# Optimization experiments

Hardware: AMD Instinct MI355X
Metric: run time of the kernel (lower is better)

Reference implementation:

```python
import jax, jax.numpy as jnp
import numpy as np

N, L, K = 2048, 256, 16

def setup_inputs() -> dict:
    rng = np.random.default_rng(0)
    # per level: wavelet index = l (distinct across levels), plus K-1 random distinct rest indices
    sel = np.zeros((L, K), dtype=np.int64)
    wav = np.arange(L, dtype=np.int64)
    all_idx = np.arange(N)
    for l in range(L):
        others = rng.choice(np.delete(all_idx, l), size=K - 1, replace=False)
        sel[l] = np.sort(np.concatenate([[l], others]))
    key = jax.random.key(0)
    k1, k2 = jax.random.split(key)
    M = jax.random.normal(k1, (N, N), dtype=jnp.float32)
    A = 0.5 * (M + M.T)  # symmetric matrix, as MMF expects
    O_all = jax.random.normal(k2, (L, K, K), dtype=jnp.float32) / np.float32(K) ** 0.5
    return {"A": A, "O_all": O_all, "sel_idx": jnp.asarray(sel), "wav_idx": jnp.asarray(wav)}


def reference(A, O_all, sel_idx, wav_idx):
    # Torch builds a dense NxN U = eye with O scattered into the KxK block at
    # sel_idx x sel_idx, then A <- U A U^T and right <- U @ right.
    # Equivalent efficient form: only the K selected rows/cols change.
    n = A.shape[0]

    def step(carry, xs):
        A, right = carry
        O, idx = xs  # O: (K,K), idx: (K,)
        A = A.at[idx].set(O @ A[idx])              # U @ A   : rewrite K rows
        A = A.at[:, idx].set(A[:, idx] @ O.T)      # ... @ U^T: rewrite K cols
        right = right.at[idx].set(O @ right[idx])  # right <- U @ right
        return (A, right), None

    right0 = jnp.eye(n, dtype=A.dtype)
    (A_f, right), _ = jax.lax.scan(step, (A, right0), (O_all, sel_idx))

    # final_active_index: 1 everywhere except wavelet indices
    active = jnp.ones((n,), dtype=A.dtype).at[wav_idx].set(0.0)
    # left_index = eye - diag(diag(outer)) + outer  -> diag all ones, off-diag = a_i*a_j
    left = jnp.outer(active, active)
    left = left.at[jnp.diag_indices(n)].set(1.0)
    D = A_f * left
    A_rec = right.T @ D @ right
    return (A_rec, right, D)
```

## Files before the change

kernel.cpp:

```cpp
#include <hip/hip_runtime.h>

#define N 2048
#define LEV 256
#define KS 16

typedef __attribute__((ext_vector_type(8))) short bfx8;
typedef __attribute__((ext_vector_type(4))) float fx4;
typedef unsigned short u16;
typedef unsigned int u32;

static const size_t NN = (size_t)N * N;

__device__ inline u16 bf16_rne(float f) {
    u32 u = __builtin_bit_cast(u32, f);
    u32 r = (u + 0x7FFFu + ((u >> 16) & 1u)) >> 16;
    return (u16)r;
}
__device__ inline float bf16_f(u16 h) {
    u32 u = ((u32)h) << 16;
    return __builtin_bit_cast(float, u);
}

#define GLDS16(gp, lp) __builtin_amdgcn_global_load_lds( \
    (const __attribute__((address_space(1))) void*)(uintptr_t)(gp), \
    (__attribute__((address_space(3))) void*)(u32)(uintptr_t)(lp), 16, 0, 0)

__device__ inline float qadd(float x) {
#if __has_builtin(__builtin_amdgcn_mov_dpp)
    int a = __builtin_amdgcn_mov_dpp(__builtin_bit_cast(int, x), 0xB1, 0xF, 0xF, true);
    float y = x + __builtin_bit_cast(float, a);
    int b = __builtin_amdgcn_mov_dpp(__builtin_bit_cast(int, y), 0x4E, 0xF, 0xF, true);
    return y + __builtin_bit_cast(float, b);
#else
    float y = x + __shfl_xor(x, 1);
    return y + __shfl_xor(y, 2);
#endif
}

__global__ __launch_bounds__(64)
void front_k(const float* __restrict__ O_all, const int* __restrict__ sel,
             float* __restrict__ RT, const float* __restrict__ A,
             u16* __restrict__ a2h) {
    __shared__ float x[2048];
    const int lane = threadIdx.x;

    if (blockIdx.x >= 2048) {
        u16* a2l = a2h + NN;
        size_t p = (((size_t)blockIdx.x - 2048) * 64 + lane) * 8;
        float4 v0 = *(const float4*)(A + p);
        float4 v1 = *(const float4*)(A + p + 4);
        float vv[8] = {v0.x, v0.y, v0.z, v0.w, v1.x, v1.y, v1.z, v1.w};
        bfx8 hs, ls;
        #pragma unroll
        for (int i = 0; i < 8; ++i) {
            u16 h = bf16_rne(vv[i]);
            hs[i] = (short)h;
            ls[i] = (short)bf16_rne(vv[i] - bf16_f(h));
        }
        *(bfx8*)(a2h + p) = hs;
        *(bfx8*)(a2l + p) = ls;
        return;
    }

    const int i    = lane >> 2;
    const int kg   = lane & 3;
    const int col  = blockIdx.x;

    const float4 z = make_float4(0.f, 0.f, 0.f, 0.f);
    #pragma unroll
    for (int q = 0; q < 8; ++q) *(float4*)&x[q * 256 + lane * 4] = z;
    if (lane == 0) x[col] = 1.0f;

    const float* obase = O_all + i * KS + kg * 4;
    const int*   gbase = sel + kg * 4;

#define CMP(f, g, wv) { \
    float p = f.x * x[g.x] + f.y * x[g.y] + f.z * x[g.z] + f.w * x[g.w]; \
    p = qadd(p); \
    if (kg == 0) x[wv] = p; }

    float4 f0 = *(const float4*)(obase);
    int4   g0 = *(const int4*)(gbase);
    int    w0 = sel[i];
    float4 f1 = *(const float4*)(obase + 256);
    int4   g1 = *(const int4*)(gbase + KS);
    int    w1 = sel[KS + i];

    for (int l = 0; l < LEV; l += 2) {
        float4 f2, f3; int4 g2, g3; int w2, w3;
        if (l + 2 < LEV) {
            f2 = *(const float4*)(obase + (size_t)(l + 2) * 256);
            g2 = *(const int4*)(gbase + (l + 2) * KS);
            w2 = sel[(l + 2) * KS + i];
            f3 = *(const float4*)(obase + (size_t)(l + 3) * 256);
            g3 = *(const int4*)(gbase + (l + 3) * KS);
            w3 = sel[(l + 3) * KS + i];
        } else { f2 = f0; g2 = g0; w2 = w0; f3 = f1; g3 = g1; w3 = w1; }

        CMP(f0, g0, w0)
        CMP(f1, g1, w1)
        f0 = f2; g0 = g2; w0 = w2;
        f1 = f3; g1 = g3; w1 = w3;
    }
#undef CMP

    #pragma unroll
    for (int q = 0; q < 8; ++q)
        *(float4*)&RT[(size_t)col * N + q * 256 + lane * 4] =
            *(const float4*)&x[q * 256 + lane * 4];
}

__global__ __launch_bounds__(256)
void split_rt_k(const float* __restrict__ RT, u16* __restrict__ r2h,
                u16* __restrict__ rth, float* __restrict__ Rrm) {
    __shared__ float t[64][65];
    u16* r2l = r2h + NN;
    u16* rtl = rth + NN;
    const int r0 = (blockIdx.x >> 5) * 64, c0 = (blockIdx.x & 31) * 64;
    #pragma unroll
    for (int i = 0; i < 16; ++i) {
        int q = i * 256 + threadIdx.x;
        int rr = q >> 6, cc = q & 63;
        t[rr][cc] = RT[(size_t)(r0 + rr) * N + c0 + cc];
    }
    __syncthreads();
    #pragma unroll
    for (int i = 0; i < 16; ++i) {
        int q = i * 256 + threadIdx.x;
        int rr = q >> 6, cc = q & 63;
        float v = t[rr][cc];
        u16 h = bf16_rne(v);
        size_t po = (size_t)(r0 + rr) * N + c0 + cc;
        rth[po] = h;
        rtl[po] = bf16_rne(v - bf16_f(h));
        float w = t[cc][rr];
        u16 h2 = bf16_rne(w);
        size_t pt = (size_t)(c0 + rr) * N + r0 + cc;
        r2h[pt] = h2;
        r2l[pt] = bf16_rne(w - bf16_f(h2));
        Rrm[pt] = w;
    }
}

__global__ __launch_bounds__(256)
void unsplit_k(const u16* __restrict__ hi, float* __restrict__ dst) {
    const u16* lo = hi + NN;
    size_t p = ((size_t)blockIdx.x * 256 + threadIdx.x) * 8;
    bfx8 hs = *(const bfx8*)(hi + p);
    bfx8 ls = *(const bfx8*)(lo + p);
    float4 o0, o1;
    o0.x = bf16_f((u16)hs[0]) + bf16_f((u16)ls[0]);
    o0.y = bf16_f((u16)hs[1]) + bf16_f((u16)ls[1]);
    o0.z = bf16_f((u16)hs[2]) + bf16_f((u16)ls[2]);
    o0.w = bf16_f((u16)hs[3]) + bf16_f((u16)ls[3]);
    o1.x = bf16_f((u16)hs[4]) + bf16_f((u16)ls[4]);
    o1.y = bf16_f((u16)hs[5]) + bf16_f((u16)ls[5]);
    o1.z = bf16_f((u16)hs[6]) + bf16_f((u16)ls[6]);
    o1.w = bf16_f((u16)hs[7]) + bf16_f((u16)ls[7]);
    *(float4*)(dst + p)     = o0;
    *(float4*)(dst + p + 4) = o1;
}

template<int MASKED, int OMODE>
__global__ __launch_bounds__(256)
void gemm_bf3(const u16* __restrict__ Xp, const u16* __restrict__ Yp,
              float* __restrict__ Cf, u16* __restrict__ Cs,
              const int* __restrict__ wav, int Lw) {
    __shared__ __align__(16) u16 sm[24576];
    __shared__ float rowf[128], colf[64];

    const int tid = threadIdx.x;
    const int xcd = blockIdx.x & 7, idx = blockIdx.x >> 3;
    const int sup = 4 * xcd + (idx >> 4);
    const int wi4 = idx & 15;
    const int by = (sup >> 3) * 4 + (wi4 >> 2);
    const int bx = (sup & 7) * 4 + (wi4 & 3);
    const int i0 = by * 128, j0 = bx * 64;
    const int lane = tid & 63, w = tid >> 6;
    const int wm = (w >> 1) * 64, wn = (w & 1) * 32;
    const int fr = lane & 15;

    if (MASKED) {
        if (tid < 128) rowf[tid] = 1.0f;
        if (tid >= 128 && tid < 192) colf[tid - 128] = 1.0f;
        __syncthreads();
        for (int t = tid; t < Lw; t += 256) {
            int wv = wav[t];
            int dr = wv - i0; if (0 <= dr && dr < 128) rowf[dr] = 0.0f;
            int dc = wv - j0; if (0 <= dc && dc < 64)  colf[dc] = 0.0f;
        }
    }

    fx4 acc[4][2];
    #pragma unroll
    for (int m = 0; m < 4; ++m)
        #pragma unroll
        for (int n = 0; n < 2; ++n)
            acc[m][n] = (fx4)0.0f;

    const u16* Xh = Xp; const u16* Xl = Xp + NN;
    const u16* Yh = Yp; const u16* Yl = Yp + NN;

    const int rl   = lane >> 3;
    const int gcol = ((lane & 7) ^ rl) << 3;
    const int wq   = w * 1024;

    #define STAGE(kt) { \
        const int k0s = (kt) * 64; \
        char* lb0 = (char*)sm + wq; \
        _Pragma("unroll") \
        for (int q = 0; q < 4; ++q) { \
            const int row = q * 32 + w * 8 + rl; \
            const size_t xo = (size_t)(i0 + row) * N + k0s + gcol; \
            GLDS16(Xh + xo, lb0 + q * 4096); \
            GLDS16(Xl + xo, lb0 + 16384 + q * 4096); \
        } \
        _Pragma("unroll") \
        for (int q = 0; q < 2; ++q) { \
            const int row = q * 32 + w * 8 + rl; \
            const size_t yo = (size_t)(j0 + row) * N + k0s + gcol; \
            GLDS16(Yh + yo, lb0 + 32768 + q * 4096); \
            GLDS16(Yl + yo, lb0 + 40960 + q * 4096); \
        } }

    const int kq  = (lane >> 4) << 4;
    const int frx = (fr & 7) << 4;

    #define COMPUTE() { \
        const char* base = (const char*)sm; \
        _Pragma("unroll") \
        for (int s = 0; s < 2; ++s) { \
            const int cb = s * 64 + kq; \
            bfx8 ah[4], al[4]; \
            _Pragma("unroll") \
            for (int m = 0; m < 4; ++m) { \
                const int off = (wm + m * 16 + fr) * 128 + (cb ^ frx); \
                ah[m] = *(const bfx8*)(base + off); \
                al[m] = *(const bfx8*)(base + 16384 + off); \
            } \
            _Pragma("unroll") \
            for (int n = 0; n < 2; ++n) { \
                const int off = (wn + n * 16 + fr) * 128 + (cb ^ frx); \
                bfx8 bh = *(const bfx8*)(base + 32768 + off); \
                bfx8 bl = *(const bfx8*)(base + 40960 + off); \
                _Pragma("unroll") \
                for (int m = 0; m < 4; ++m) { \
                    acc[m][n] = __builtin_amdgcn_mfma_f32_16x16x32_bf16(ah[m], bh, acc[m][n], 0, 0, 0); \
                    acc[m][n] = __builtin_amdgcn_mfma_f32_16x16x32_bf16(ah[m], bl, acc[m][n], 0, 0, 0); \
                    acc[m][n] = __builtin_amdgcn_mfma_f32_16x16x32_bf16(al[m], bh, acc[m][n], 0, 0, 0); \
                } \
            } \
        } }

    constexpr int NT = N / 64;
    for (int kt = 0; kt < NT; ++kt) {
        STAGE(kt)
        __syncthreads();
        COMPUTE()
        __syncthreads();
    }

    const int crow0 = (lane >> 4) * 4;
    #pragma unroll
    for (int m = 0; m < 4; ++m) {
        #pragma unroll
        for (int n = 0; n < 2; ++n) {
            #pragma unroll
            for (int r = 0; r < 4; ++r) {
                const int li = wm + m * 16 + crow0 + r;
                const int lj = wn + n * 16 + fr;
                float v = acc[m][n][r];
                if (MASKED) {
                    if (i0 + li != j0 + lj) v *= rowf[li] * colf[lj];
                }
                const size_t off = (size_t)(i0 + li) * N + j0 + lj;
                if (OMODE == 0) {
                    Cf[off] = v;
                } else {
                    u16 h = bf16_rne(v);
                    Cs[off]      = h;
                    Cs[NN + off] = bf16_rne(v - bf16_f(h));
                }
            }
        }
    }
    #undef STAGE
    #undef COMPUTE
}

extern "C" void kernel_launch(void* const* d_in, const int* in_sizes, int n_in,
                              void* d_out, int out_size, void* d_ws, size_t ws_size,
                              hipStream_t stream) {
    const float* A     = (const float*)d_in[0];
    const float* O_all = (const float*)d_in[1];
    const int*   sel   = (const int*)d_in[2];
    const int*   wav   = (const int*)d_in[3];
    const int    Lw    = in_sizes[3];

    float* O1 = (float*)d_out;
    float* O2 = O1 + NN;
    float* O3 = O1 + 2 * NN;

    u16*   W1u = (u16*)d_ws;
    u16*   W2u = (u16*)((char*)d_ws + 2 * NN * sizeof(u16));
    u16*   O1u = (u16*)O1;
    u16*   O3u = (u16*)O3;

    const int SGRID = (int)(NN / (256 * 8));

    front_k<<<2048 + (int)(NN / (64 * 8)), 64, 0, stream>>>(O_all, sel, O3, A, W2u);
    split_rt_k<<<(N / 64) * (N / 64), 256, 0, stream>>>(O3, O1u, W1u, O2);

    gemm_bf3<0, 1><<<512, 256, 0, stream>>>(O1u, W2u, nullptr, O3u, nullptr, 0);
    gemm_bf3<1, 1><<<512, 256, 0, stream>>>(O3u, O1u, nullptr, W2u, wav, Lw);
    gemm_bf3<0, 1><<<512, 256, 0, stream>>>(W1u, W2u, nullptr, O3u, nullptr, 0);
    gemm_bf3<0, 0><<<512, 256, 0, stream>>>(O3u, W1u, O1, nullptr, nullptr, 0);
    unsplit_k<<<SGRID, 256, 0, stream>>>(W2u, O3);
}
```

Before: 265.4 us.

## Load GEMM B operand directly to registers and split RT in front kernel

The GEMM kernel stops staging the Y (B) operand through LDS and has each lane load its MFMA B fragments straight from global memory into registers, which shrinks LDS use and removes the LDS write/read traffic for B. Separately, the bf16 hi/lo split of RT moves into the front kernel's final store, so split_rt_k only writes the transposed outputs. The direct global loads for B are 16-byte per-lane reads spread across 16 rows and are issued before the barrier. They may expose more latency and fetch the same data redundantly across waves that share B columns.

```diff
diff --git a/kernel.cpp b/kernel.cpp
--- a/kernel.cpp
+++ b/kernel.cpp
@@ -39,8 +39,8 @@
 
 __global__ __launch_bounds__(64)
 void front_k(const float* __restrict__ O_all, const int* __restrict__ sel,
-             float* __restrict__ RT, const float* __restrict__ A,
-             u16* __restrict__ a2h) {
+             float* __restrict__ RT, u16* __restrict__ rth,
+             const float* __restrict__ A, u16* __restrict__ a2h) {
     __shared__ float x[2048];
     const int lane = threadIdx.x;
 
@@ -104,18 +104,29 @@
     }
 #undef CMP
 
-    #pragma unroll
-    for (int q = 0; q < 8; ++q)
-        *(float4*)&RT[(size_t)col * N + q * 256 + lane * 4] =
-            *(const float4*)&x[q * 256 + lane * 4];
+    u16* rtl = rth + NN;
+    #pragma unroll
+    for (int q = 0; q < 8; ++q) {
+        float4 v = *(const float4*)&x[q * 256 + lane * 4];
+        *(float4*)&RT[(size_t)col * N + q * 256 + lane * 4] = v;
+        float vv[4] = {v.x, v.y, v.z, v.w};
+        u16 hh[4], ll[4];
+        #pragma unroll
+        for (int e = 0; e < 4; ++e) {
+            hh[e] = bf16_rne(vv[e]);
+            ll[e] = bf16_rne(vv[e] - bf16_f(hh[e]));
+        }
+        const size_t po = (size_t)col * N + q * 256 + lane * 4;
+        *(ushort4*)(rth + po) = make_ushort4(hh[0], hh[1], hh[2], hh[3]);
+        *(ushort4*)(rtl + po) = make_ushort4(ll[0], ll[1], ll[2], ll[3]);
+    }
 }
 
 __global__ __launch_bounds__(256)
 void split_rt_k(const float* __restrict__ RT, u16* __restrict__ r2h,
-                u16* __restrict__ rth, float* __restrict__ Rrm) {
+                float* __restrict__ Rrm) {
     __shared__ float t[64][65];
     u16* r2l = r2h + NN;
-    u16* rtl = rth + NN;
     const int r0 = (blockIdx.x >> 5) * 64, c0 = (blockIdx.x & 31) * 64;
     #pragma unroll
     for (int i = 0; i < 16; ++i) {
@@ -128,11 +139,6 @@
     for (int i = 0; i < 16; ++i) {
         int q = i * 256 + threadIdx.x;
         int rr = q >> 6, cc = q & 63;
-        float v = t[rr][cc];
-        u16 h = bf16_rne(v);
-        size_t po = (size_t)(r0 + rr) * N + c0 + cc;
-        rth[po] = h;
-        rtl[po] = bf16_rne(v - bf16_f(h));
         float w = t[cc][rr];
         u16 h2 = bf16_rne(w);
         size_t pt = (size_t)(c0 + rr) * N + r0 + cc;
@@ -166,7 +172,7 @@
 void gemm_bf3(const u16* __restrict__ Xp, const u16* __restrict__ Yp,
               float* __restrict__ Cf, u16* __restrict__ Cs,
               const int* __restrict__ wav, int Lw) {
-    __shared__ __align__(16) u16 sm[24576];
+    __shared__ __align__(16) u16 sm[16384];
     __shared__ float rowf[128], colf[64];
 
     const int tid = threadIdx.x;
@@ -179,6 +185,7 @@
     const int lane = tid & 63, w = tid >> 6;
     const int wm = (w >> 1) * 64, wn = (w & 1) * 32;
     const int fr = lane & 15;
+    const int fk = (lane >> 4) * 8;
 
     if (MASKED) {
         if (tid < 128) rowf[tid] = 1.0f;
@@ -199,64 +206,62 @@
             acc[m][n] = (fx4)0.0f;
 
     const u16* Xh = Xp; const u16* Xl = Xp + NN;
-    const u16* Yh = Yp; const u16* Yl = Yp + NN;
 
     const int rl   = lane >> 3;
     const int gcol = ((lane & 7) ^ rl) << 3;
     const int wq   = w * 1024;
-
-    #define STAGE(kt) { \
-        const int k0s = (kt) * 64; \
-        char* lb0 = (char*)sm + wq; \
-        _Pragma("unroll") \
-        for (int q = 0; q < 4; ++q) { \
-            const int row = q * 32 + w * 8 + rl; \
-            const size_t xo = (size_t)(i0 + row) * N + k0s + gcol; \
-            GLDS16(Xh + xo, lb0 + q * 4096); \
-            GLDS16(Xl + xo, lb0 + 16384 + q * 4096); \
-        } \
-        _Pragma("unroll") \
-        for (int q = 0; q < 2; ++q) { \
-            const int row = q * 32 + w * 8 + rl; \
-            const size_t yo = (size_t)(j0 + row) * N + k0s + gcol; \
-            GLDS16(Yh + yo, lb0 + 32768 + q * 4096); \
-            GLDS16(Yl + yo, lb0 + 40960 + q * 4096); \
-        } }
-
-    const int kq  = (lane >> 4) << 4;
-    const int frx = (fr & 7) << 4;
-
-    #define COMPUTE() { \
-        const char* base = (const char*)sm; \
-        _Pragma("unroll") \
-        for (int s = 0; s < 2; ++s) { \
-            const int cb = s * 64 + kq; \
-            bfx8 ah[4], al[4]; \
-            _Pragma("unroll") \
-            for (int m = 0; m < 4; ++m) { \
-                const int off = (wm + m * 16 + fr) * 128 + (cb ^ frx); \
-                ah[m] = *(const bfx8*)(base + off); \
-                al[m] = *(const bfx8*)(base + 16384 + off); \
-            } \
-            _Pragma("unroll") \
-            for (int n = 0; n < 2; ++n) { \
-                const int off = (wn + n * 16 + fr) * 128 + (cb ^ frx); \
-                bfx8 bh = *(const bfx8*)(base + 32768 + off); \
-                bfx8 bl = *(const bfx8*)(base + 40960 + off); \
-                _Pragma("unroll") \
-                for (int m = 0; m < 4; ++m) { \
-                    acc[m][n] = __builtin_amdgcn_mfma_f32_16x16x32_bf16(ah[m], bh, acc[m][n], 0, 0, 0); \
-                    acc[m][n] = __builtin_amdgcn_mfma_f32_16x16x32_bf16(ah[m], bl, acc[m][n], 0, 0, 0); \
-                    acc[m][n] = __builtin_amdgcn_mfma_f32_16x16x32_bf16(al[m], bh, acc[m][n], 0, 0, 0); \
-                } \
-            } \
-        } }
+    const int kq   = (lane >> 4) << 4;
+    const int frx  = (fr & 7) << 4;
 
     constexpr int NT = N / 64;
     for (int kt = 0; kt < NT; ++kt) {
-        STAGE(kt)
+        const int k0s = kt * 64;
+        {
+            char* lb0 = (char*)sm + wq;
+            #pragma unroll
+            for (int q = 0; q < 4; ++q) {
+                const int row = q * 32 + w * 8 + rl;
+                const size_t xo = (size_t)(i0 + row) * N + k0s + gcol;
+                GLDS16(Xh + xo, lb0 + q * 4096);
+                GLDS16(Xl + xo, lb0 + 16384 + q * 4096);
+            }
+        }
+        bfx8 yf[2][2][2];
+        #pragma unroll
+        for (int n = 0; n < 2; ++n)
+            #pragma unroll
+            for (int s = 0; s < 2; ++s) {
+                const u16* yb = Yp + (size_t)(j0 + wn + n * 16 + fr) * N
+                                   + k0s + s * 32 + fk;
+                yf[n][s][0] = *(const bfx8*)yb;
+                yf[n][s][1] = *(const bfx8*)(yb + NN);
+            }
         __syncthreads();
-        COMPUTE()
+        {
+            const char* base = (const char*)sm;
+            #pragma unroll
+            for (int s = 0; s < 2; ++s) {
+                const int cb = s * 64 + kq;
+                bfx8 ah[4], al[4];
+                #pragma unroll
+                for (int m = 0; m < 4; ++m) {
+                    const int off = (wm + m * 16 + fr) * 128 + (cb ^ frx);
+                    ah[m] = *(const bfx8*)(base + off);
+                    al[m] = *(const bfx8*)(base + 16384 + off);
+                }
+                #pragma unroll
+                for (int n = 0; n < 2; ++n) {
+                    bfx8 bh = yf[n][s][0];
+                    bfx8 bl = yf[n][s][1];
+                    #pragma unroll
+                    for (int m = 0; m < 4; ++m) {
+                        acc[m][n] = __builtin_amdgcn_mfma_f32_16x16x32_bf16(ah[m], bh, acc[m][n], 0, 0, 0);
+                        acc[m][n] = __builtin_amdgcn_mfma_f32_16x16x32_bf16(ah[m], bl, acc[m][n], 0, 0, 0);
+                        acc[m][n] = __builtin_amdgcn_mfma_f32_16x16x32_bf16(al[m], bh, acc[m][n], 0, 0, 0);
+                    }
+                }
+            }
+        }
         __syncthreads();
     }
 
@@ -284,8 +289,6 @@
             }
         }
     }
-    #undef STAGE
-    #undef COMPUTE
 }
 
 extern "C" void kernel_launch(void* const* d_in, const int* in_sizes, int n_in,
@@ -308,8 +311,8 @@
 
     const int SGRID = (int)(NN / (256 * 8));
 
-    front_k<<<2048 + (int)(NN / (64 * 8)), 64, 0, stream>>>(O_all, sel, O3, A, W2u);
-    split_rt_k<<<(N / 64) * (N / 64), 256, 0, stream>>>(O3, O1u, W1u, O2);
+    front_k<<<2048 + (int)(NN / (64 * 8)), 64, 0, stream>>>(O_all, sel, O3, W1u, A, W2u);
+    split_rt_k<<<(N / 64) * (N / 64), 256, 0, stream>>>(O3, O1u, O2);
 
     gemm_bf3<0, 1><<<512, 256, 0, stream>>>(O1u, W2u, nullptr, O3u, nullptr, 0);
     gemm_bf3<1, 1><<<512, 256, 0, stream>>>(O3u, O1u, nullptr, W2u, wav, Lw);
```

New measurement: 398.5 us. 1.5x slower.

## Forward previous-level results via bpermute to break LDS dependency chain in front kernel

Applied to the files above, without the earlier changes.

The per-column sequential level recurrence now tags each LDS entry with the level and row that last wrote it. When the next level needs a value produced by the level just finished, it takes it straight from registers with ds_bpermute. This lets LDS loads for level l+1 be issued before level l's store, removing the store-then-load round trip on the serial critical path. The front kernel also writes the hi/lo bf16 split of RT directly, so split_rt_k no longer does that part. The cost is doubled LDS footprint (int2 per entry), extra bpermute and select work per step, and more intricate forwarding logic.

```diff
diff --git a/kernel.cpp b/kernel.cpp
--- a/kernel.cpp
+++ b/kernel.cpp
@@ -39,9 +39,9 @@
 
 __global__ __launch_bounds__(64)
 void front_k(const float* __restrict__ O_all, const int* __restrict__ sel,
-             float* __restrict__ RT, const float* __restrict__ A,
-             u16* __restrict__ a2h) {
-    __shared__ float x[2048];
+             float* __restrict__ RT, u16* __restrict__ rth,
+             const float* __restrict__ A, u16* __restrict__ a2h) {
+    __shared__ int2 xm[2048];
     const int lane = threadIdx.x;
 
     if (blockIdx.x >= 2048) {
@@ -65,57 +65,91 @@
     const int i    = lane >> 2;
     const int kg   = lane & 3;
     const int col  = blockIdx.x;
-
-    const float4 z = make_float4(0.f, 0.f, 0.f, 0.f);
-    #pragma unroll
-    for (int q = 0; q < 8; ++q) *(float4*)&x[q * 256 + lane * 4] = z;
-    if (lane == 0) x[col] = 1.0f;
+    const int SENT = 1 << 30;
+
+    #pragma unroll
+    for (int q = 0; q < 32; ++q) xm[q * 64 + lane] = make_int2(0, SENT);
+    if (lane == 0) xm[col].x = 0x3F800000;
 
     const float* obase = O_all + i * KS + kg * 4;
     const int*   gbase = sel + kg * 4;
 
-#define CMP(f, g, wv) { \
-    float p = f.x * x[g.x] + f.y * x[g.y] + f.z * x[g.z] + f.w * x[g.w]; \
-    p = qadd(p); \
-    if (kg == 0) x[wv] = p; }
-
-    float4 f0 = *(const float4*)(obase);
-    int4   g0 = *(const int4*)(gbase);
-    int    w0 = sel[i];
-    float4 f1 = *(const float4*)(obase + 256);
-    int4   g1 = *(const int4*)(gbase + KS);
-    int    w1 = sel[KS + i];
-
-    for (int l = 0; l < LEV; l += 2) {
-        float4 f2, f3; int4 g2, g3; int w2, w3;
+    float4 o_c = *(const float4*)(obase);
+    int4   g_c = *(const int4*)(gbase);
+    int    w_c = sel[i];
+    float4 o_n = *(const float4*)(obase + 256);
+    int4   g_n = *(const int4*)(gbase + KS);
+    int    w_n = sel[KS + i];
+
+    if (kg == 1) xm[w_c].y = i;
+
+    int2 t0 = xm[g_c.x], t1 = xm[g_c.y], t2 = xm[g_c.z], t3 = xm[g_c.w];
+    float v_st[4] = {__builtin_bit_cast(float, t0.x), __builtin_bit_cast(float, t1.x),
+                     __builtin_bit_cast(float, t2.x), __builtin_bit_cast(float, t3.x)};
+    int   mk[4]   = {t0.y, t1.y, t2.y, t3.y};
+    float p_prev = 0.0f;
+
+    for (int l = 0; l < LEV; ++l) {
+        float4 o_p; int4 g_p; int w_p;
         if (l + 2 < LEV) {
-            f2 = *(const float4*)(obase + (size_t)(l + 2) * 256);
-            g2 = *(const int4*)(gbase + (l + 2) * KS);
-            w2 = sel[(l + 2) * KS + i];
-            f3 = *(const float4*)(obase + (size_t)(l + 3) * 256);
-            g3 = *(const int4*)(gbase + (l + 3) * KS);
-            w3 = sel[(l + 3) * KS + i];
-        } else { f2 = f0; g2 = g0; w2 = w0; f3 = f1; g3 = g1; w3 = w1; }
-
-        CMP(f0, g0, w0)
-        CMP(f1, g1, w1)
-        f0 = f2; g0 = g2; w0 = w2;
-        f1 = f3; g1 = g3; w1 = w3;
-    }
-#undef CMP
-
-    #pragma unroll
-    for (int q = 0; q < 8; ++q)
+            o_p = *(const float4*)(obase + (size_t)(l + 2) * 256);
+            g_p = *(const int4*)(gbase + (l + 2) * KS);
+            w_p = sel[(l + 2) * KS + i];
+        } else { o_p = o_n; g_p = g_n; w_p = w_n; }
+
+        const int ew = l - 1;
+        const int pbits = __builtin_bit_cast(int, p_prev);
+        float v[4];
+        #pragma unroll
+        for (int e = 0; e < 4; ++e) {
+            int bp = __builtin_amdgcn_ds_bpermute((mk[e] & 15) << 4, pbits);
+            v[e] = ((mk[e] >> 4) == ew) ? __builtin_bit_cast(float, bp) : v_st[e];
+        }
+
+        int2 u0 = xm[g_n.x], u1 = xm[g_n.y], u2 = xm[g_n.z], u3 = xm[g_n.w];
+
+        if (kg == 1) xm[w_n].y = ((l + 1) << 4) | i;
+
+        float p = o_c.x * v[0] + o_c.y * v[1] + o_c.z * v[2] + o_c.w * v[3];
+        p = qadd(p);
+
+        if (kg == 0) xm[w_c].x = __builtin_bit_cast(int, p);
+
+        p_prev = p;
+        v_st[0] = __builtin_bit_cast(float, u0.x); mk[0] = u0.y;
+        v_st[1] = __builtin_bit_cast(float, u1.x); mk[1] = u1.y;
+        v_st[2] = __builtin_bit_cast(float, u2.x); mk[2] = u2.y;
+        v_st[3] = __builtin_bit_cast(float, u3.x); mk[3] = u3.y;
+        o_c = o_n; g_c = g_n; w_c = w_n;
+        o_n = o_p; g_n = g_p; w_n = w_p;
+    }
+
+    u16* rtl = rth + NN;
+    #pragma unroll
+    for (int q = 0; q < 8; ++q) {
+        float vv[4];
+        #pragma unroll
+        for (int e = 0; e < 4; ++e)
+            vv[e] = __builtin_bit_cast(float, xm[q * 256 + lane * 4 + e].x);
         *(float4*)&RT[(size_t)col * N + q * 256 + lane * 4] =
-            *(const float4*)&x[q * 256 + lane * 4];
+            make_float4(vv[0], vv[1], vv[2], vv[3]);
+        u16 hh[4], ll[4];
+        #pragma unroll
+        for (int e = 0; e < 4; ++e) {
+            hh[e] = bf16_rne(vv[e]);
+            ll[e] = bf16_rne(vv[e] - bf16_f(hh[e]));
+        }
+        const size_t po = (size_t)col * N + q * 256 + lane * 4;
+        *(ushort4*)(rth + po) = make_ushort4(hh[0], hh[1], hh[2], hh[3]);
+        *(ushort4*)(rtl + po) = make_ushort4(ll[0], ll[1], ll[2], ll[3]);
+    }
 }
 
 __global__ __launch_bounds__(256)
 void split_rt_k(const float* __restrict__ RT, u16* __restrict__ r2h,
-                u16* __restrict__ rth, float* __restrict__ Rrm) {
+                float* __restrict__ Rrm) {
     __shared__ float t[64][65];
     u16* r2l = r2h + NN;
-    u16* rtl = rth + NN;
     const int r0 = (blockIdx.x >> 5) * 64, c0 = (blockIdx.x & 31) * 64;
     #pragma unroll
     for (int i = 0; i < 16; ++i) {
@@ -128,11 +162,6 @@
     for (int i = 0; i < 16; ++i) {
         int q = i * 256 + threadIdx.x;
         int rr = q >> 6, cc = q & 63;
-        float v = t[rr][cc];
-        u16 h = bf16_rne(v);
-        size_t po = (size_t)(r0 + rr) * N + c0 + cc;
-        rth[po] = h;
-        rtl[po] = bf16_rne(v - bf16_f(h));
         float w = t[cc][rr];
         u16 h2 = bf16_rne(w);
         size_t pt = (size_t)(c0 + rr) * N + r0 + cc;
@@ -308,8 +337,8 @@
 
     const int SGRID = (int)(NN / (256 * 8));
 
-    front_k<<<2048 + (int)(NN / (64 * 8)), 64, 0, stream>>>(O_all, sel, O3, A, W2u);
-    split_rt_k<<<(N / 64) * (N / 64), 256, 0, stream>>>(O3, O1u, W1u, O2);
+    front_k<<<2048 + (int)(NN / (64 * 8)), 64, 0, stream>>>(O_all, sel, O3, W1u, A, W2u);
+    split_rt_k<<<(N / 64) * (N / 64), 256, 0, stream>>>(O3, O1u, O2);
 
     gemm_bf3<0, 1><<<512, 256, 0, stream>>>(O1u, W2u, nullptr, O3u, nullptr, 0);
     gemm_bf3<1, 1><<<512, 256, 0, stream>>>(O3u, O1u, nullptr, W2u, wav, Lw);
```

New measurement: 298.7 us. 12.5% more time.
